# Kernel optimization log

Measured on AMD Instinct MI355X. Metric: run time of the kernel, lower is better.

The kernel has to match this reference:

```python
import jax, jax.numpy as jnp
import numpy as np

EMBED_SIZE = 100
HEAD_SIZE = 64
B, T = 4, 4096


def setup_inputs() -> dict:
    key = jax.random.key(0)
    k1, k2, k3, k4 = jax.random.split(key, 4)
    x = jax.random.normal(k1, (B, T, EMBED_SIZE), dtype=jnp.float32)
    Wq = jax.random.normal(k2, (EMBED_SIZE, HEAD_SIZE), dtype=jnp.float32) * 0.1
    Wk = jax.random.normal(k3, (EMBED_SIZE, HEAD_SIZE), dtype=jnp.float32) * 0.1
    Wv = jax.random.normal(k4, (EMBED_SIZE, HEAD_SIZE), dtype=jnp.float32) * 0.1
    return {"x": x, "Wq": Wq, "Wk": Wk, "Wv": Wv}


def reference(x, Wq, Wk, Wv):
    # Projections (bias-free Linear): [B, T, head_size]
    q = x @ Wq
    k = x @ Wk
    v = x @ Wv
    scale = HEAD_SIZE ** (-0.5)
    # Scaled scores [B, T, T]
    scores = jnp.einsum("bqd,bkd->bqk", q, k) * scale
    # Faithful to source: tril the scores, then mask entries that equal 0 to -inf
    masked = jnp.tril(scores)
    masked = jnp.where(masked == 0, -jnp.inf, masked)
    attn = jax.nn.softmax(masked, axis=-1)
    out = jnp.einsum("bqk,bkd->bqd", attn, v)  # [B, T, head_size]
    return out
```

## Files before the change

### kernel.cpp

```cpp
#include <hip/hip_runtime.h>
#include <hip/hip_bf16.h>
#include <stdint.h>

#define NB 4
#define NT 4096
#define NE 100
#define ND 64

typedef __attribute__((ext_vector_type(8))) short short8;
typedef __attribute__((ext_vector_type(4))) short short4_;
typedef __attribute__((ext_vector_type(4))) float float4_;
typedef unsigned short ushort_t;

__device__ __forceinline__ unsigned short f2bf(float f) {
  union { float f; uint32_t u; } v; v.f = f;
  uint32_t u = v.u;
  u += 0x7fffu + ((u >> 16) & 1u);
  return (unsigned short)(u >> 16);
}

__device__ __forceinline__ float bf2f(short us) {
  union { uint32_t u; float f; } v;
  v.u = ((uint32_t)(unsigned short)us) << 16;
  return v.f;
}

__device__ __forceinline__ float fast_exp2(float x) {
#if __has_builtin(__builtin_amdgcn_exp2f)
  return __builtin_amdgcn_exp2f(x);
#else
  return exp2f(x);
#endif
}

__global__ __launch_bounds__(256) void proj_kernel(
    const float* __restrict__ x, const float* __restrict__ Wq,
    const float* __restrict__ Wk, const float* __restrict__ Wv,
    ushort_t* __restrict__ Qb, ushort_t* __restrict__ Kb,
    ushort_t* __restrict__ Vt) {
  __shared__ __align__(16) float xs[64 * NE];
  __shared__ __align__(16) ushort_t Wl[3][25][64][4];
  __shared__ __align__(16) ushort_t Vl[64][72];

  const int tid = threadIdx.x;
  const int r0  = blockIdx.x * 64;

  {
    const float4_* xsrc = (const float4_*)(x + (size_t)r0 * NE);
    float4_* xdst = (float4_*)xs;
    for (int i = tid; i < 1600; i += 256) xdst[i] = xsrc[i];
  }
  {
    const int ch = tid >> 6, d = tid & 63;
    if (ch < 3) {
      const float* Ws = (ch == 0) ? Wq : (ch == 1) ? Wk : Wv;
      #pragma unroll 5
      for (int qd = 0; qd < 25; ++qd) {
        short4_ pk;
        #pragma unroll
        for (int jj = 0; jj < 4; ++jj)
          pk[jj] = (short)f2bf(Ws[(4*qd + jj)*ND + d]);
        *(short4_*)&Wl[ch][qd][d][0] = pk;
      }
    }
  }
  __syncthreads();

  const int wv = tid >> 6, lane = tid & 63;
  const float QS = 0.125f * 1.44269504088896340736f;

  for (int it = 0; it < 4; ++it) {
    float aq[4] = {0,0,0,0}, ak[4] = {0,0,0,0}, av[4] = {0,0,0,0};
    const float* xw = xs + (it*16 + wv*4) * NE;
    for (int qd = 0; qd < 25; ++qd) {
      short4_ w4q = *(const short4_*)&Wl[0][qd][lane][0];
      short4_ w4k = *(const short4_*)&Wl[1][qd][lane][0];
      short4_ w4v = *(const short4_*)&Wl[2][qd][lane][0];
      float4_ x0 = *(const float4_*)&xw[0*NE + 4*qd];
      float4_ x1 = *(const float4_*)&xw[1*NE + 4*qd];
      float4_ x2 = *(const float4_*)&xw[2*NE + 4*qd];
      float4_ x3 = *(const float4_*)&xw[3*NE + 4*qd];
      #pragma unroll
      for (int jj = 0; jj < 4; ++jj) {
        float fq = bf2f(w4q[jj]), fk = bf2f(w4k[jj]), fv = bf2f(w4v[jj]);
        aq[0] += x0[jj]*fq; ak[0] += x0[jj]*fk; av[0] += x0[jj]*fv;
        aq[1] += x1[jj]*fq; ak[1] += x1[jj]*fk; av[1] += x1[jj]*fv;
        aq[2] += x2[jj]*fq; ak[2] += x2[jj]*fk; av[2] += x2[jj]*fv;
        aq[3] += x3[jj]*fq; ak[3] += x3[jj]*fk; av[3] += x3[jj]*fv;
      }
    }
    #pragma unroll
    for (int j = 0; j < 4; ++j) {
      int lrow = it*16 + wv*4 + j;
      int row  = r0 + lrow;
      Qb[(size_t)row*ND + lane] = f2bf(aq[j] * QS);
      Kb[(size_t)row*ND + lane] = f2bf(ak[j]);
      Vl[lrow][lane] = f2bf(av[j]);
    }
  }
  __syncthreads();

  {
    const int b = r0 >> 12, r0t = r0 & (NT - 1);
    for (int i = tid; i < 512; i += 256) {
      int d = i >> 3, seg = i & 7;
      short8 pk;
      #pragma unroll
      for (int k2 = 0; k2 < 8; ++k2) pk[k2] = (short)Vl[seg*8 + k2][d];
      *(short8*)(Vt + ((size_t)(b*ND + d))*NT + r0t + seg*8) = pk;
    }
  }
}

__global__ __launch_bounds__(512, 2) void attn_kernel(
    const ushort_t* __restrict__ Qb, const ushort_t* __restrict__ Kb,
    const ushort_t* __restrict__ Vt, float* __restrict__ out) {
  __shared__ __align__(16) ushort_t Pb[8][16][72];
  __shared__ __align__(16) float Om[8][16][64];
  __shared__ float Ml[8][16][2];

  const int tid  = threadIdx.x;
  const int w    = tid >> 6, lane = tid & 63;
  const int pp   = w >> 1, h = w & 1;
  const int qrow = lane & 15, grp = lane >> 4;

  const int blk = blockIdx.x;
  const int xcd = blk & 7;
  const int b   = xcd >> 1;
  const int p   = ((blk >> 3) << 1) | (xcd & 1);

  const ushort_t* Kbase = Kb + (size_t)b*NT*ND;
  const ushort_t* Vtb   = Vt + (size_t)b*ND*NT;
  ushort_t* Pw = &Pb[w][0][0];

  for (int phase = 0; phase < 2; ++phase) {
    const int g  = phase ? p : (127 - p);
    const int q0 = g << 5;
    const int nt = (g >> 1) + 1;
    const int qglob = q0 + h*16 + qrow;

    const ushort_t* Qr = Qb + ((size_t)(b*NT + q0 + h*16 + qrow))*ND + 8*grp;
    const short8 qf0 = *(const short8*)(Qr);
    const short8 qf1 = *(const short8*)(Qr + 32);

    float4_ O0 = {0,0,0,0}, O1 = {0,0,0,0}, O2 = {0,0,0,0}, O3 = {0,0,0,0};
    float m = -1e30f, lsum = 0.f;
    short8 kc[8], kn[8];

    const int maxIter = (nt + 3) >> 2;

    if (pp < nt) {
      const int kv0 = pp << 6;
      #pragma unroll
      for (int st = 0; st < 4; ++st) {
        const ushort_t* kp = Kbase + (size_t)(kv0 + st*16 + qrow)*ND + 8*grp;
        kc[2*st]   = *(const short8*)(kp);
        kc[2*st+1] = *(const short8*)(kp + 32);
      }
    }
    #pragma unroll
    for (int i = 0; i < 8; ++i) kn[i] = kc[i];

    for (int it = 0; it < maxIter; ++it) {
      const int t   = pp + (it << 2);
      const bool act = (t < nt);
      if (act) {
        const int kv0 = t << 6;

        short8 vf[8];
        #pragma unroll
        for (int j = 0; j < 4; ++j) {
          const ushort_t* vp = Vtb + (size_t)(j*16 + qrow)*NT + kv0 + 8*grp;
          vf[2*j]   = *(const short8*)(vp);
          vf[2*j+1] = *(const short8*)(vp + 32);
        }
        if (t + 4 < nt) {
          const int kn0 = (t + 4) << 6;
          #pragma unroll
          for (int st = 0; st < 4; ++st) {
            const ushort_t* kp = Kbase + (size_t)(kn0 + st*16 + qrow)*ND + 8*grp;
            kn[2*st]   = *(const short8*)(kp);
            kn[2*st+1] = *(const short8*)(kp + 32);
          }
        }

        float4_ sA[4];
        #pragma unroll
        for (int st = 0; st < 4; ++st) {
          float4_ acc = {0,0,0,0};
          acc = __builtin_amdgcn_mfma_f32_16x16x32_bf16(kc[2*st],   qf0, acc, 0,0,0);
          acc = __builtin_amdgcn_mfma_f32_16x16x32_bf16(kc[2*st+1], qf1, acc, 0,0,0);
          sA[st] = acc;
        }

        if (t == nt - 1) {
          #pragma unroll
          for (int st = 0; st < 4; ++st)
            #pragma unroll
            for (int r = 0; r < 4; ++r) {
              int kv = kv0 + st*16 + grp*4 + r;
              if (kv > qglob) sA[st][r] = -1e30f;
            }
        }

        float pmax = sA[0][0];
        #pragma unroll
        for (int st = 0; st < 4; ++st)
          #pragma unroll
          for (int r = 0; r < 4; ++r) pmax = fmaxf(pmax, sA[st][r]);
        if (!__all(pmax <= m + 8.0f)) {
          float tm = pmax;
          tm = fmaxf(tm, __shfl_xor(tm, 16));
          tm = fmaxf(tm, __shfl_xor(tm, 32));
          const float mnew  = fmaxf(m, tm);
          const float alpha = fast_exp2(m - mnew);
          m = mnew;
          lsum *= alpha;
          #pragma unroll
          for (int r = 0; r < 4; ++r) {
            float ar = __shfl(alpha, grp*4 + r);
            O0[r] *= ar; O1[r] *= ar; O2[r] *= ar; O3[r] *= ar;
          }
        }

        float ps0 = 0.f, ps1 = 0.f;
        #pragma unroll
        for (int st = 0; st < 4; ++st) {
          short4_ pv;
          float pe0 = fast_exp2(sA[st][0] - m);
          float pe1 = fast_exp2(sA[st][1] - m);
          float pe2 = fast_exp2(sA[st][2] - m);
          float pe3 = fast_exp2(sA[st][3] - m);
          pv[0] = (short)f2bf(pe0); pv[1] = (short)f2bf(pe1);
          pv[2] = (short)f2bf(pe2); pv[3] = (short)f2bf(pe3);
          ps0 += pe0 + pe1; ps1 += pe2 + pe3;
          *(short4_*)&Pw[qrow*72 + st*16 + grp*4] = pv;
        }
        lsum += ps0 + ps1;

        asm volatile("s_waitcnt lgkmcnt(0)" ::: "memory");

        const short8 pf0 = *(const short8*)&Pw[qrow*72 + 8*grp];
        const short8 pf1 = *(const short8*)&Pw[qrow*72 + 32 + 8*grp];
        O0 = __builtin_amdgcn_mfma_f32_16x16x32_bf16(pf0, vf[0], O0, 0,0,0);
        O0 = __builtin_amdgcn_mfma_f32_16x16x32_bf16(pf1, vf[1], O0, 0,0,0);
        O1 = __builtin_amdgcn_mfma_f32_16x16x32_bf16(pf0, vf[2], O1, 0,0,0);
        O1 = __builtin_amdgcn_mfma_f32_16x16x32_bf16(pf1, vf[3], O1, 0,0,0);
        O2 = __builtin_amdgcn_mfma_f32_16x16x32_bf16(pf0, vf[4], O2, 0,0,0);
        O2 = __builtin_amdgcn_mfma_f32_16x16x32_bf16(pf1, vf[5], O2, 0,0,0);
        O3 = __builtin_amdgcn_mfma_f32_16x16x32_bf16(pf0, vf[6], O3, 0,0,0);
        O3 = __builtin_amdgcn_mfma_f32_16x16x32_bf16(pf1, vf[7], O3, 0,0,0);

        #pragma unroll
        for (int i = 0; i < 8; ++i) kc[i] = kn[i];
      }
    }

    lsum += __shfl_xor(lsum, 16);
    lsum += __shfl_xor(lsum, 32);

    #pragma unroll
    for (int r = 0; r < 4; ++r) {
      int row = grp*4 + r;
      Om[w][row][0*16 + qrow] = O0[r];
      Om[w][row][1*16 + qrow] = O1[r];
      Om[w][row][2*16 + qrow] = O2[r];
      Om[w][row][3*16 + qrow] = O3[r];
    }
    if (lane < 16) {
      Ml[w][lane][0] = m;
      Ml[w][lane][1] = lsum;
    }
    __syncthreads();

    for (int i = tid; i < 2048; i += 512) {
      int row = i >> 6, d = i & 63;
      int hh = row >> 4, r16 = row & 15;
      float M = -3e30f;
      #pragma unroll
      for (int p2 = 0; p2 < 4; ++p2)
        M = fmaxf(M, Ml[2*p2 + hh][r16][0]);
      float ls = 0.f, os = 0.f;
      #pragma unroll
      for (int p2 = 0; p2 < 4; ++p2) {
        int w2 = 2*p2 + hh;
        float sc = fast_exp2(Ml[w2][r16][0] - M);
        ls += sc * Ml[w2][r16][1];
        os += sc * Om[w2][r16][d];
      }
      out[((size_t)b*NT + q0 + row)*ND + d] = os / ls;
    }
    __syncthreads();
  }
}

extern "C" void kernel_launch(void* const* d_in, const int* in_sizes, int n_in,
                              void* d_out, int out_size, void* d_ws, size_t ws_size,
                              hipStream_t stream) {
  const float* x  = (const float*)d_in[0];
  const float* Wq = (const float*)d_in[1];
  const float* Wk = (const float*)d_in[2];
  const float* Wv = (const float*)d_in[3];
  float* out = (float*)d_out;

  ushort_t* Qb = (ushort_t*)d_ws;
  ushort_t* Kb = Qb + (size_t)NB*NT*ND;
  ushort_t* Vt = Kb + (size_t)NB*NT*ND;

  proj_kernel<<<dim3(256), dim3(256), 0, stream>>>(x, Wq, Wk, Wv, Qb, Kb, Vt);
  attn_kernel<<<dim3(256), dim3(512), 0, stream>>>(Qb, Kb, Vt, out);
}
```

Measured before the change: 148.8 us.

## Split attention into one query tile per block, tile V layout, raise occupancy

The attention kernel now launches 512 blocks with one 32-row query tile each, replacing 256 blocks that each walked two paired tiles (long plus short). Heavy tiles are ordered first to balance causal work, and launch bounds now allow four blocks per CU. V is stored in 64x64 tiles per KV block so each tile is a contiguous 8 KB chunk. K double-buffer prefetch is removed to save registers, and packed bf16 conversion uses v_cvt_pk_bf16_f32. The cost is less load-latency hiding within a wave, traded for more waves resident per CU.

```diff
diff --git a/kernel.cpp b/kernel.cpp
--- a/kernel.cpp
+++ b/kernel.cpp
@@ -33,11 +33,17 @@
 #endif
 }
 
+__device__ __forceinline__ uint32_t cvtpk_bf16(float a, float b) {
+  uint32_t r;
+  asm("v_cvt_pk_bf16_f32 %0, %1, %2" : "=v"(r) : "v"(a), "v"(b));
+  return r;
+}
+
 __global__ __launch_bounds__(256) void proj_kernel(
     const float* __restrict__ x, const float* __restrict__ Wq,
     const float* __restrict__ Wk, const float* __restrict__ Wv,
     ushort_t* __restrict__ Qb, ushort_t* __restrict__ Kb,
-    ushort_t* __restrict__ Vt) {
+    ushort_t* __restrict__ Vp) {
   __shared__ __align__(16) float xs[64 * NE];
   __shared__ __align__(16) ushort_t Wl[3][25][64][4];
   __shared__ __align__(16) ushort_t Vl[64][72];
@@ -102,19 +108,20 @@
 
   {
     const int b = r0 >> 12, r0t = r0 & (NT - 1);
+    ushort_t* Vdst = Vp + (size_t)b*NT*ND + (size_t)(r0t >> 6)*4096;
     for (int i = tid; i < 512; i += 256) {
       int d = i >> 3, seg = i & 7;
       short8 pk;
       #pragma unroll
       for (int k2 = 0; k2 < 8; ++k2) pk[k2] = (short)Vl[seg*8 + k2][d];
-      *(short8*)(Vt + ((size_t)(b*ND + d))*NT + r0t + seg*8) = pk;
-    }
-  }
-}
-
-__global__ __launch_bounds__(512, 2) void attn_kernel(
+      *(short8*)(Vdst + d*64 + seg*8) = pk;
+    }
+  }
+}
+
+__global__ __launch_bounds__(512, 4) void attn_kernel(
     const ushort_t* __restrict__ Qb, const ushort_t* __restrict__ Kb,
-    const ushort_t* __restrict__ Vt, float* __restrict__ out) {
+    const ushort_t* __restrict__ Vp, float* __restrict__ out) {
   __shared__ __align__(16) ushort_t Pb[8][16][72];
   __shared__ __align__(16) float Om[8][16][64];
   __shared__ float Ml[8][16][2];
@@ -127,170 +134,143 @@
   const int blk = blockIdx.x;
   const int xcd = blk & 7;
   const int b   = xcd >> 1;
-  const int p   = ((blk >> 3) << 1) | (xcd & 1);
+  const int par = xcd & 1;
+  const int u   = blk >> 3;
+  const int g = (u < 32) ? (127 - (2*u + par)) : ((u - 32)*2 + par);
+
+  const int q0 = g << 5;
+  const int nt = (g >> 1) + 1;
+  const int qglob = q0 + h*16 + qrow;
 
   const ushort_t* Kbase = Kb + (size_t)b*NT*ND;
-  const ushort_t* Vtb   = Vt + (size_t)b*ND*NT;
+  const ushort_t* Vpb   = Vp + (size_t)b*NT*ND;
   ushort_t* Pw = &Pb[w][0][0];
 
-  for (int phase = 0; phase < 2; ++phase) {
-    const int g  = phase ? p : (127 - p);
-    const int q0 = g << 5;
-    const int nt = (g >> 1) + 1;
-    const int qglob = q0 + h*16 + qrow;
-
-    const ushort_t* Qr = Qb + ((size_t)(b*NT + q0 + h*16 + qrow))*ND + 8*grp;
-    const short8 qf0 = *(const short8*)(Qr);
-    const short8 qf1 = *(const short8*)(Qr + 32);
-
-    float4_ O0 = {0,0,0,0}, O1 = {0,0,0,0}, O2 = {0,0,0,0}, O3 = {0,0,0,0};
-    float m = -1e30f, lsum = 0.f;
-    short8 kc[8], kn[8];
-
-    const int maxIter = (nt + 3) >> 2;
-
-    if (pp < nt) {
-      const int kv0 = pp << 6;
-      #pragma unroll
-      for (int st = 0; st < 4; ++st) {
-        const ushort_t* kp = Kbase + (size_t)(kv0 + st*16 + qrow)*ND + 8*grp;
-        kc[2*st]   = *(const short8*)(kp);
-        kc[2*st+1] = *(const short8*)(kp + 32);
+  const ushort_t* Qr = Qb + ((size_t)(b*NT + q0 + h*16 + qrow))*ND + 8*grp;
+  const short8 qf0 = *(const short8*)(Qr);
+  const short8 qf1 = *(const short8*)(Qr + 32);
+
+  float4_ O0 = {0,0,0,0}, O1 = {0,0,0,0}, O2 = {0,0,0,0}, O3 = {0,0,0,0};
+  float m = -1e30f, lsum = 0.f;
+
+  for (int t = pp; t < nt; t += 4) {
+    const int kv0 = t << 6;
+
+    short8 kc[8];
+    #pragma unroll
+    for (int st = 0; st < 4; ++st) {
+      const ushort_t* kp = Kbase + (size_t)(kv0 + st*16 + qrow)*ND + 8*grp;
+      kc[2*st]   = *(const short8*)(kp);
+      kc[2*st+1] = *(const short8*)(kp + 32);
+    }
+
+    float4_ sA[4];
+    #pragma unroll
+    for (int st = 0; st < 4; ++st) {
+      float4_ acc = {0,0,0,0};
+      acc = __builtin_amdgcn_mfma_f32_16x16x32_bf16(kc[2*st],   qf0, acc, 0,0,0);
+      acc = __builtin_amdgcn_mfma_f32_16x16x32_bf16(kc[2*st+1], qf1, acc, 0,0,0);
+      sA[st] = acc;
+    }
+
+    if (t == nt - 1) {
+      #pragma unroll
+      for (int st = 0; st < 4; ++st)
+        #pragma unroll
+        for (int r = 0; r < 4; ++r) {
+          int kv = kv0 + st*16 + grp*4 + r;
+          if (kv > qglob) sA[st][r] = -1e30f;
+        }
+    }
+
+    float pmax = sA[0][0];
+    #pragma unroll
+    for (int st = 0; st < 4; ++st)
+      #pragma unroll
+      for (int r = 0; r < 4; ++r) pmax = fmaxf(pmax, sA[st][r]);
+    if (!__all(pmax <= m + 8.0f)) {
+      float tm = pmax;
+      tm = fmaxf(tm, __shfl_xor(tm, 16));
+      tm = fmaxf(tm, __shfl_xor(tm, 32));
+      const float mnew  = fmaxf(m, tm);
+      const float alpha = fast_exp2(m - mnew);
+      m = mnew;
+      lsum *= alpha;
+      #pragma unroll
+      for (int r = 0; r < 4; ++r) {
+        float ar = __shfl(alpha, grp*4 + r);
+        O0[r] *= ar; O1[r] *= ar; O2[r] *= ar; O3[r] *= ar;
       }
     }
-    #pragma unroll
-    for (int i = 0; i < 8; ++i) kn[i] = kc[i];
-
-    for (int it = 0; it < maxIter; ++it) {
-      const int t   = pp + (it << 2);
-      const bool act = (t < nt);
-      if (act) {
-        const int kv0 = t << 6;
-
-        short8 vf[8];
-        #pragma unroll
-        for (int j = 0; j < 4; ++j) {
-          const ushort_t* vp = Vtb + (size_t)(j*16 + qrow)*NT + kv0 + 8*grp;
-          vf[2*j]   = *(const short8*)(vp);
-          vf[2*j+1] = *(const short8*)(vp + 32);
-        }
-        if (t + 4 < nt) {
-          const int kn0 = (t + 4) << 6;
-          #pragma unroll
-          for (int st = 0; st < 4; ++st) {
-            const ushort_t* kp = Kbase + (size_t)(kn0 + st*16 + qrow)*ND + 8*grp;
-            kn[2*st]   = *(const short8*)(kp);
-            kn[2*st+1] = *(const short8*)(kp + 32);
-          }
-        }
-
-        float4_ sA[4];
-        #pragma unroll
-        for (int st = 0; st < 4; ++st) {
-          float4_ acc = {0,0,0,0};
-          acc = __builtin_amdgcn_mfma_f32_16x16x32_bf16(kc[2*st],   qf0, acc, 0,0,0);
-          acc = __builtin_amdgcn_mfma_f32_16x16x32_bf16(kc[2*st+1], qf1, acc, 0,0,0);
-          sA[st] = acc;
-        }
-
-        if (t == nt - 1) {
-          #pragma unroll
-          for (int st = 0; st < 4; ++st)
-            #pragma unroll
-            for (int r = 0; r < 4; ++r) {
-              int kv = kv0 + st*16 + grp*4 + r;
-              if (kv > qglob) sA[st][r] = -1e30f;
-            }
-        }
-
-        float pmax = sA[0][0];
-        #pragma unroll
-        for (int st = 0; st < 4; ++st)
-          #pragma unroll
-          for (int r = 0; r < 4; ++r) pmax = fmaxf(pmax, sA[st][r]);
-        if (!__all(pmax <= m + 8.0f)) {
-          float tm = pmax;
-          tm = fmaxf(tm, __shfl_xor(tm, 16));
-          tm = fmaxf(tm, __shfl_xor(tm, 32));
-          const float mnew  = fmaxf(m, tm);
-          const float alpha = fast_exp2(m - mnew);
-          m = mnew;
-          lsum *= alpha;
-          #pragma unroll
-          for (int r = 0; r < 4; ++r) {
-            float ar = __shfl(alpha, grp*4 + r);
-            O0[r] *= ar; O1[r] *= ar; O2[r] *= ar; O3[r] *= ar;
-          }
-        }
-
-        float ps0 = 0.f, ps1 = 0.f;
-        #pragma unroll
-        for (int st = 0; st < 4; ++st) {
-          short4_ pv;
-          float pe0 = fast_exp2(sA[st][0] - m);
-          float pe1 = fast_exp2(sA[st][1] - m);
-          float pe2 = fast_exp2(sA[st][2] - m);
-          float pe3 = fast_exp2(sA[st][3] - m);
-          pv[0] = (short)f2bf(pe0); pv[1] = (short)f2bf(pe1);
-          pv[2] = (short)f2bf(pe2); pv[3] = (short)f2bf(pe3);
-          ps0 += pe0 + pe1; ps1 += pe2 + pe3;
-          *(short4_*)&Pw[qrow*72 + st*16 + grp*4] = pv;
-        }
-        lsum += ps0 + ps1;
-
-        asm volatile("s_waitcnt lgkmcnt(0)" ::: "memory");
-
-        const short8 pf0 = *(const short8*)&Pw[qrow*72 + 8*grp];
-        const short8 pf1 = *(const short8*)&Pw[qrow*72 + 32 + 8*grp];
-        O0 = __builtin_amdgcn_mfma_f32_16x16x32_bf16(pf0, vf[0], O0, 0,0,0);
-        O0 = __builtin_amdgcn_mfma_f32_16x16x32_bf16(pf1, vf[1], O0, 0,0,0);
-        O1 = __builtin_amdgcn_mfma_f32_16x16x32_bf16(pf0, vf[2], O1, 0,0,0);
-        O1 = __builtin_amdgcn_mfma_f32_16x16x32_bf16(pf1, vf[3], O1, 0,0,0);
-        O2 = __builtin_amdgcn_mfma_f32_16x16x32_bf16(pf0, vf[4], O2, 0,0,0);
-        O2 = __builtin_amdgcn_mfma_f32_16x16x32_bf16(pf1, vf[5], O2, 0,0,0);
-        O3 = __builtin_amdgcn_mfma_f32_16x16x32_bf16(pf0, vf[6], O3, 0,0,0);
-        O3 = __builtin_amdgcn_mfma_f32_16x16x32_bf16(pf1, vf[7], O3, 0,0,0);
-
-        #pragma unroll
-        for (int i = 0; i < 8; ++i) kc[i] = kn[i];
-      }
-    }
-
-    lsum += __shfl_xor(lsum, 16);
-    lsum += __shfl_xor(lsum, 32);
-
-    #pragma unroll
-    for (int r = 0; r < 4; ++r) {
-      int row = grp*4 + r;
-      Om[w][row][0*16 + qrow] = O0[r];
-      Om[w][row][1*16 + qrow] = O1[r];
-      Om[w][row][2*16 + qrow] = O2[r];
-      Om[w][row][3*16 + qrow] = O3[r];
-    }
-    if (lane < 16) {
-      Ml[w][lane][0] = m;
-      Ml[w][lane][1] = lsum;
-    }
-    __syncthreads();
-
-    for (int i = tid; i < 2048; i += 512) {
-      int row = i >> 6, d = i & 63;
-      int hh = row >> 4, r16 = row & 15;
-      float M = -3e30f;
-      #pragma unroll
-      for (int p2 = 0; p2 < 4; ++p2)
-        M = fmaxf(M, Ml[2*p2 + hh][r16][0]);
-      float ls = 0.f, os = 0.f;
-      #pragma unroll
-      for (int p2 = 0; p2 < 4; ++p2) {
-        int w2 = 2*p2 + hh;
-        float sc = fast_exp2(Ml[w2][r16][0] - M);
-        ls += sc * Ml[w2][r16][1];
-        os += sc * Om[w2][r16][d];
-      }
-      out[((size_t)b*NT + q0 + row)*ND + d] = os / ls;
-    }
-    __syncthreads();
+
+    #pragma unroll
+    for (int st = 0; st < 4; ++st) {
+      float pe0 = fast_exp2(sA[st][0] - m);
+      float pe1 = fast_exp2(sA[st][1] - m);
+      float pe2 = fast_exp2(sA[st][2] - m);
+      float pe3 = fast_exp2(sA[st][3] - m);
+      lsum += (pe0 + pe1) + (pe2 + pe3);
+      uint2 pk;
+      pk.x = cvtpk_bf16(pe0, pe1);
+      pk.y = cvtpk_bf16(pe2, pe3);
+      *(uint2*)&Pw[qrow*72 + st*16 + grp*4] = pk;
+    }
+
+    short8 vf[8];
+    #pragma unroll
+    for (int j = 0; j < 4; ++j) {
+      const ushort_t* vp = Vpb + (size_t)t*4096 + (j*16 + qrow)*64 + grp*8;
+      vf[2*j]   = *(const short8*)(vp);
+      vf[2*j+1] = *(const short8*)(vp + 32);
+    }
+
+    asm volatile("s_waitcnt lgkmcnt(0)" ::: "memory");
+
+    const short8 pf0 = *(const short8*)&Pw[qrow*72 + 8*grp];
+    const short8 pf1 = *(const short8*)&Pw[qrow*72 + 32 + 8*grp];
+    O0 = __builtin_amdgcn_mfma_f32_16x16x32_bf16(pf0, vf[0], O0, 0,0,0);
+    O0 = __builtin_amdgcn_mfma_f32_16x16x32_bf16(pf1, vf[1], O0, 0,0,0);
+    O1 = __builtin_amdgcn_mfma_f32_16x16x32_bf16(pf0, vf[2], O1, 0,0,0);
+    O1 = __builtin_amdgcn_mfma_f32_16x16x32_bf16(pf1, vf[3], O1, 0,0,0);
+    O2 = __builtin_amdgcn_mfma_f32_16x16x32_bf16(pf0, vf[4], O2, 0,0,0);
+    O2 = __builtin_amdgcn_mfma_f32_16x16x32_bf16(pf1, vf[5], O2, 0,0,0);
+    O3 = __builtin_amdgcn_mfma_f32_16x16x32_bf16(pf0, vf[6], O3, 0,0,0);
+    O3 = __builtin_amdgcn_mfma_f32_16x16x32_bf16(pf1, vf[7], O3, 0,0,0);
+  }
+
+  lsum += __shfl_xor(lsum, 16);
+  lsum += __shfl_xor(lsum, 32);
+
+  #pragma unroll
+  for (int r = 0; r < 4; ++r) {
+    int row = grp*4 + r;
+    Om[w][row][0*16 + qrow] = O0[r];
+    Om[w][row][1*16 + qrow] = O1[r];
+    Om[w][row][2*16 + qrow] = O2[r];
+    Om[w][row][3*16 + qrow] = O3[r];
+  }
+  if (lane < 16) {
+    Ml[w][lane][0] = m;
+    Ml[w][lane][1] = lsum;
+  }
+  __syncthreads();
+
+  for (int i = tid; i < 2048; i += 512) {
+    int row = i >> 6, d = i & 63;
+    int hh = row >> 4, r16 = row & 15;
+    float M = -3e30f;
+    #pragma unroll
+    for (int p2 = 0; p2 < 4; ++p2)
+      M = fmaxf(M, Ml[2*p2 + hh][r16][0]);
+    float ls = 0.f, os = 0.f;
+    #pragma unroll
+    for (int p2 = 0; p2 < 4; ++p2) {
+      int w2 = 2*p2 + hh;
+      float sc = fast_exp2(Ml[w2][r16][0] - M);
+      ls += sc * Ml[w2][r16][1];
+      os += sc * Om[w2][r16][d];
+    }
+    out[((size_t)b*NT + q0 + row)*ND + d] = os / ls;
   }
 }
 
@@ -305,8 +285,8 @@
 
   ushort_t* Qb = (ushort_t*)d_ws;
   ushort_t* Kb = Qb + (size_t)NB*NT*ND;
-  ushort_t* Vt = Kb + (size_t)NB*NT*ND;
-
-  proj_kernel<<<dim3(256), dim3(256), 0, stream>>>(x, Wq, Wk, Wv, Qb, Kb, Vt);
-  attn_kernel<<<dim3(256), dim3(512), 0, stream>>>(Qb, Kb, Vt, out);
-}
+  ushort_t* Vp = Kb + (size_t)NB*NT*ND;
+
+  proj_kernel<<<dim3(256), dim3(256), 0, stream>>>(x, Wq, Wk, Wv, Qb, Kb, Vp);
+  attn_kernel<<<dim3(512), dim3(512), 0, stream>>>(Qb, Kb, Vp, out);
+}
```

Measured after the change: 149.3 us. Within noise of the previous version (+0.3%).
